# Optimization experiments

Measured on AMD Instinct MI355X. Metric: run time of the kernel, lower is better.

## Reference

```python
import jax, jax.numpy as jnp
import numpy as np

N = 30000      # nodes
E = 240000     # edges (before self-loops)
D = 128        # vec_dim
L = 6          # GAT layers
NEG_SLOPE = 0.2
EPS = 1e-5


def setup_inputs() -> dict:
    key = jax.random.key(0)
    ks = jax.random.split(key, 20)
    s = 1.0 / np.sqrt(D)
    inp = {
        "x": jax.random.randint(ks[0], (N,), 0, 120),
        "edge_index": jax.random.randint(ks[1], (2, E), 0, N),
        "emb": jax.random.normal(ks[2], (120, D), jnp.float32) * 0.05,
        # stacked GATv2Conv params for 6 layers (heads=1)
        "Wl": jax.random.normal(ks[3], (L, D, D), jnp.float32) * s,
        "bl": jnp.zeros((L, D), jnp.float32),
        "Wr": jax.random.normal(ks[4], (L, D, D), jnp.float32) * s,
        "br": jnp.zeros((L, D), jnp.float32),
        "att": jax.random.normal(ks[5], (L, D), jnp.float32) * s,
        "conv_bias": jnp.zeros((L, D), jnp.float32),
        # PyG LayerNorm (applied after layers 0..4)
        "ln_g": jnp.ones((L - 1, D), jnp.float32),
        "ln_b": jnp.zeros((L - 1, D), jnp.float32),
        # outer Linear + BatchNorm1d
        "lin_W": jax.random.normal(ks[6], (D, D), jnp.float32) * s,
        "lin_b": jnp.zeros((D,), jnp.float32),
        "bn_g": jnp.ones((D,), jnp.float32),
        "bn_b": jnp.zeros((D,), jnp.float32),
    }
    return inp


def _segment_softmax(score, seg, num_segments):
    # numerically stable softmax over variable-degree neighborhoods
    m = jax.ops.segment_max(score, seg, num_segments=num_segments)
    ex = jnp.exp(score - m[seg])
    denom = jax.ops.segment_sum(ex, seg, num_segments=num_segments)
    return ex / denom[seg]


def _gat_forward(h, src, dst, Wl, bl, Wr, br, att, conv_bias, ln_g, ln_b):
    xg = h
    for i in range(L):
        xl = xg @ Wl[i] + bl[i]          # [N, D] source transform
        xr = xg @ Wr[i] + br[i]          # [N, D] target transform
        # GATv2 attention: a^T LeakyReLU(x_l[j] + x_r[i]) per edge j->i
        e = jax.nn.leaky_relu(xl[src] + xr[dst], NEG_SLOPE)   # [E2, D]
        score = e @ att[i]                                     # [E2]
        alpha = _segment_softmax(score, dst, N)                # [E2]
        msg = alpha[:, None] * xl[src]                         # [E2, D]
        xg = jax.ops.segment_sum(msg, dst, num_segments=N) + conv_bias[i]
        if i < L - 1:
            # PyG LayerNorm(mode='graph'): global mean/std, per-channel affine
            mu = xg.mean()
            var = ((xg - mu) ** 2).mean()
            xg = (xg - mu) / jnp.sqrt(var + EPS) * ln_g[i] + ln_b[i]
            xg = jax.nn.relu(xg)
            # dropout(0.1) is identity in eval mode
    return xg


def reference(x, edge_index, emb, Wl, bl, Wr, br, att, conv_bias,
              ln_g, ln_b, lin_W, lin_b, bn_g, bn_b):
    h = emb[x]                                      # [N, D]
    # PyG GATv2Conv default add_self_loops=True
    loops = jnp.arange(N, dtype=edge_index.dtype)
    src = jnp.concatenate([edge_index[0], loops])   # [E2]
    dst = jnp.concatenate([edge_index[1], loops])   # [E2]
    xg = _gat_forward(h, src, dst, Wl, bl, Wr, br, att, conv_bias, ln_g, ln_b)
    out = (h + xg) @ lin_W + lin_b                  # [N, D]
    # BatchNorm1d (batch-statistics / train-mode math)
    mu = out.mean(axis=0)
    var = out.var(axis=0)
    out = (out - mu) / jnp.sqrt(var + EPS) * bn_g + bn_b
    return out
```

## Files before the change

### kernel.cpp

```cpp
#include <hip/hip_runtime.h>
#include <math.h>

#define N_NODES 30000
#define N_EDGES 240000
#define E2 (N_EDGES + N_NODES)
#define D 128
#define LAYERS 6
#define NEG_SLOPE 0.2f
#define LN_EPS 1e-5f

typedef unsigned short u16;
typedef unsigned int u32;
using bfrag = __attribute__((ext_vector_type(8))) short;
using f32x4 = __attribute__((ext_vector_type(4))) float;

__device__ inline u16 f2bf(float f) {
    u32 u = __float_as_uint(f);
    u32 r = u + 0x7fffu + ((u >> 16) & 1u);
    return (u16)(r >> 16);
}
__device__ inline u32 pack2(float a, float b) { return (u32)f2bf(a) | ((u32)f2bf(b) << 16); }
__device__ inline float bflo(u32 u) { return __uint_as_float(u << 16); }
__device__ inline float bfhi(u32 u) { return __uint_as_float(u & 0xffff0000u); }
__device__ inline u32 bfadd2(u32 a, u32 b) {
    return pack2(bflo(a) + bflo(b), bfhi(a) + bfhi(b));
}

__device__ inline float red8_dpp(float x) {
    x += __int_as_float(__builtin_amdgcn_update_dpp(0, __float_as_int(x), 0xB1, 0xF, 0xF, true));
    x += __int_as_float(__builtin_amdgcn_update_dpp(0, __float_as_int(x), 0x4E, 0xF, 0xF, true));
    x += __int_as_float(__builtin_amdgcn_update_dpp(0, __float_as_int(x), 0x141, 0xF, 0xF, true));
    return x;
}

__global__ __launch_bounds__(256) void wt_convert(const float* __restrict__ Wl,
        const float* __restrict__ Wr, const float* __restrict__ linW, u16* __restrict__ wt)
{
    __shared__ u16 tile[128 * 129];
    int b = blockIdx.x;
    const float* src = (b == 12) ? linW
                     : ((b & 1) ? Wr + (size_t)(b >> 1) * 16384 : Wl + (size_t)(b >> 1) * 16384);
    int t = threadIdx.x;
    #pragma unroll 4
    for (int i = 0; i < 64; i++) {
        int idx = t + 256 * i;
        int k = idx >> 7, n = idx & 127;
        tile[n * 129 + k] = f2bf(src[idx]);
    }
    __syncthreads();
    u16* dst = wt + (size_t)b * 16384;
    #pragma unroll 4
    for (int i = 0; i < 64; i++) {
        int idx = t + 256 * i;
        int n = idx >> 7, k = idx & 127;
        dst[idx] = tile[n * 129 + k];
    }
}

__global__ __launch_bounds__(256) void hist_kernel(const int* __restrict__ ei, int* __restrict__ cnt)
{
    int e = blockIdx.x * 256 + threadIdx.x;
    if (e >= E2) return;
    int d = (e < N_EDGES) ? ei[N_EDGES + e] : (e - N_EDGES);
    atomicAdd(&cnt[d], 1);
}

__global__ __launch_bounds__(1024) void scan1_kernel(const int* __restrict__ cnt,
        int* __restrict__ lscan, int* __restrict__ bsum)
{
    __shared__ int wtot[16];
    int t = threadIdx.x, lane = t & 63, w = t >> 6;
    int i = blockIdx.x * 1024 + t;
    int v = (i < N_NODES) ? cnt[i] : 0;
    int s = v;
    #pragma unroll
    for (int off = 1; off < 64; off <<= 1) {
        int u = __shfl_up(s, off);
        if (lane >= off) s += u;
    }
    if (lane == 63) wtot[w] = s;
    __syncthreads();
    if (t < 16) {
        int xv = wtot[t];
        #pragma unroll
        for (int off = 1; off < 16; off <<= 1) {
            int u = __shfl_up(xv, off);
            if (t >= off) xv += u;
        }
        wtot[t] = xv;
    }
    __syncthreads();
    int incl = ((w == 0) ? 0 : wtot[w - 1]) + s;
    if (i < N_NODES) lscan[i] = incl;
    if (t == 0) bsum[blockIdx.x] = wtot[15];
}

__global__ __launch_bounds__(1024) void scan3_kernel(const int* __restrict__ lscan,
        const int* __restrict__ bsum, const int* __restrict__ cnt,
        int* __restrict__ row_off, int* __restrict__ cursor)
{
    __shared__ int sboff;
    if (threadIdx.x < 64) {
        int v = (threadIdx.x < 30) ? bsum[threadIdx.x] : 0;
        int s = v;
        #pragma unroll
        for (int off = 1; off < 64; off <<= 1) {
            int u = __shfl_up(s, off);
            if ((int)threadIdx.x >= off) s += u;
        }
        if (threadIdx.x == blockIdx.x) sboff = s - v;
    }
    __syncthreads();
    int i = blockIdx.x * 1024 + threadIdx.x;
    if (i == 0) row_off[0] = 0;
    if (i < N_NODES) {
        int r = lscan[i] + sboff;
        row_off[i + 1] = r;
        cursor[i] = r - cnt[i];
    }
}

__global__ __launch_bounds__(256) void scatter_kernel(const int* __restrict__ ei,
        int* __restrict__ cursor, int* __restrict__ csr_src)
{
    int e = blockIdx.x * 256 + threadIdx.x;
    if (e >= E2) return;
    int s, d;
    if (e < N_EDGES) { s = ei[e]; d = ei[N_EDGES + e]; }
    else             { s = e - N_EDGES; d = s; }
    int pos = atomicAdd(&cursor[d], 1);
    csr_src[pos] = s;
}

template<bool LN, bool DUAL, bool OUTF, bool EMB>
__global__ __launch_bounds__(256) void gemm_mfma(
    const u16* __restrict__ Abf, const u16* __restrict__ A2bf,
    const float* __restrict__ Aln, const float* __restrict__ lnacc,
    const float* __restrict__ lng, const float* __restrict__ lnb,
    const int* __restrict__ xidx, const float* __restrict__ emb, u16* __restrict__ h_out,
    const u16* __restrict__ Wt1, const float* __restrict__ b1,
    float* __restrict__ C1f, u16* __restrict__ C1h,
    const u16* __restrict__ Wt2, const float* __restrict__ b2, u16* __restrict__ C2h,
    float* __restrict__ bnacc, int M)
{
    __shared__ u16 As[32 * 136];
    __shared__ float sLN[2];
    int t = threadIdx.x;
    int m0 = blockIdx.x * 32;
    int lane = t & 63, w = t >> 6;
    int n16 = lane & 15, quad = lane >> 4;
    int c0 = w * 32;

    bfrag bW1[2][4], bW2[2][4];
    #pragma unroll
    for (int c = 0; c < 2; c++)
        #pragma unroll
        for (int ks = 0; ks < 4; ks++)
            bW1[c][ks] = *(const bfrag*)(Wt1 + (size_t)(c0 + c * 16 + n16) * 128 + ks * 32 + quad * 8);
    if (DUAL) {
        #pragma unroll
        for (int c = 0; c < 2; c++)
            #pragma unroll
            for (int ks = 0; ks < 4; ks++)
                bW2[c][ks] = *(const bfrag*)(Wt2 + (size_t)(c0 + c * 16 + n16) * 128 + ks * 32 + quad * 8);
    }

    if (LN) {
        if (w == 0) {
            float2 v = ((const float2*)lnacc)[lane];
            float s = v.x, ss = v.y;
            #pragma unroll
            for (int off = 32; off > 0; off >>= 1) {
                s += __shfl_xor(s, off); ss += __shfl_xor(ss, off);
            }
            if (lane == 0) {
                const float invM = 1.f / ((float)N_NODES * (float)D);
                float mu  = s * invM;
                float var = ss * invM - mu * mu;
                sLN[0] = mu;
                sLN[1] = rsqrtf(var + LN_EPS);
            }
        }
        __syncthreads();
        float mu = sLN[0], inv = sLN[1];
        #pragma unroll
        for (int i = 0; i < 4; i++) {
            int idx = t + 256 * i;
            int row = idx >> 5, c4 = idx & 31;
            int gr = m0 + row;
            float4 v = make_float4(0.f, 0.f, 0.f, 0.f);
            if (gr < M) v = ((const float4*)(Aln + (size_t)gr * D))[c4];
            float4 gv = ((const float4*)lng)[c4];
            float4 bv = ((const float4*)lnb)[c4];
            v.x = (v.x - mu) * inv * gv.x + bv.x; v.x = v.x > 0.f ? v.x : 0.f;
            v.y = (v.y - mu) * inv * gv.y + bv.y; v.y = v.y > 0.f ? v.y : 0.f;
            v.z = (v.z - mu) * inv * gv.z + bv.z; v.z = v.z > 0.f ? v.z : 0.f;
            v.w = (v.w - mu) * inv * gv.w + bv.w; v.w = v.w > 0.f ? v.w : 0.f;
            uint2 pk = make_uint2(pack2(v.x, v.y), pack2(v.z, v.w));
            *(uint2*)&As[row * 136 + c4 * 4] = pk;
        }
    } else if (EMB) {
        #pragma unroll
        for (int i = 0; i < 2; i++) {
            int idx = t + 256 * i;
            int row = idx >> 4, c16 = idx & 15;
            int gr = m0 + row;
            uint4 v = make_uint4(0u, 0u, 0u, 0u);
            if (gr < M) {
                const float* er = emb + (size_t)xidx[gr] * D + c16 * 8;
                float4 e0 = ((const float4*)er)[0];
                float4 e1 = ((const float4*)er)[1];
                v.x = pack2(e0.x, e0.y); v.y = pack2(e0.z, e0.w);
                v.z = pack2(e1.x, e1.y); v.w = pack2(e1.z, e1.w);
                ((uint4*)(h_out + (size_t)gr * 128))[c16] = v;
            }
            *(uint4*)&As[row * 136 + c16 * 8] = v;
        }
    } else {
        #pragma unroll
        for (int i = 0; i < 2; i++) {
            int idx = t + 256 * i;
            int row = idx >> 4, c16 = idx & 15;
            int gr = m0 + row;
            uint4 v = make_uint4(0u, 0u, 0u, 0u);
            if (gr < M) {
                v = ((const uint4*)(Abf + (size_t)gr * 128))[c16];
                if (A2bf) {
                    uint4 u = ((const uint4*)(A2bf + (size_t)gr * 128))[c16];
                    v.x = bfadd2(v.x, u.x); v.y = bfadd2(v.y, u.y);
                    v.z = bfadd2(v.z, u.z); v.w = bfadd2(v.w, u.w);
                }
            }
            *(uint4*)&As[row * 136 + c16 * 8] = v;
        }
    }
    __syncthreads();

    f32x4 zero = {0.f, 0.f, 0.f, 0.f};
    f32x4 acc1[2][2] = {{zero, zero}, {zero, zero}};
    f32x4 acc2[2][2] = {{zero, zero}, {zero, zero}};
    #pragma unroll
    for (int ks = 0; ks < 4; ks++) {
        bfrag a[2];
        #pragma unroll
        for (int r = 0; r < 2; r++)
            a[r] = *(const bfrag*)&As[(r * 16 + n16) * 136 + ks * 32 + quad * 8];
        #pragma unroll
        for (int r = 0; r < 2; r++)
            #pragma unroll
            for (int c = 0; c < 2; c++) {
                acc1[r][c] = __builtin_amdgcn_mfma_f32_16x16x32_bf16(a[r], bW1[c][ks], acc1[r][c], 0, 0, 0);
                if (DUAL)
                    acc2[r][c] = __builtin_amdgcn_mfma_f32_16x16x32_bf16(a[r], bW2[c][ks], acc2[r][c], 0, 0, 0);
            }
    }

    float bv1[2] = { b1[c0 + n16], b1[c0 + 16 + n16] };
    float bns[2] = {0.f, 0.f}, bnss[2] = {0.f, 0.f};
    #pragma unroll
    for (int r = 0; r < 2; r++)
        #pragma unroll
        for (int c = 0; c < 2; c++)
            #pragma unroll
            for (int reg = 0; reg < 4; reg++) {
                int grow = m0 + r * 16 + quad * 4 + reg;
                if (grow < M) {
                    float val = acc1[r][c][reg] + bv1[c];
                    int col = c0 + c * 16 + n16;
                    if (OUTF) {
                        C1f[(size_t)grow * 128 + col] = val;
                        bns[c] += val; bnss[c] += val * val;
                    } else {
                        C1h[(size_t)grow * 128 + col] = f2bf(val);
                    }
                }
            }
    if (OUTF) {
        #pragma unroll
        for (int c = 0; c < 2; c++) {
            #pragma unroll
            for (int msk = 16; msk <= 32; msk <<= 1) {
                bns[c]  += __shfl_xor(bns[c], msk);
                bnss[c] += __shfl_xor(bnss[c], msk);
            }
        }
        if (quad == 0) {
            float* base = bnacc + (size_t)(blockIdx.x & 15) * 256;
            #pragma unroll
            for (int c = 0; c < 2; c++) {
                int col = c0 + c * 16 + n16;
                atomicAdd(&base[col], bns[c]);
                atomicAdd(&base[128 + col], bnss[c]);
            }
        }
    }
    if (DUAL) {
        float bv2[2] = { b2[c0 + n16], b2[c0 + 16 + n16] };
        #pragma unroll
        for (int r = 0; r < 2; r++)
            #pragma unroll
            for (int c = 0; c < 2; c++)
                #pragma unroll
                for (int reg = 0; reg < 4; reg++) {
                    int grow = m0 + r * 16 + quad * 4 + reg;
                    if (grow < M)
                        C2h[(size_t)grow * 128 + c0 + c * 16 + n16] = f2bf(acc2[r][c][reg] + bv2[c]);
                }
    }
}

__global__ __launch_bounds__(256) void gat_agg(
    const u16* __restrict__ xl, const u16* __restrict__ xr,
    const int* __restrict__ row_off, const int* __restrict__ csr_src,
    const float* __restrict__ att, const float* __restrict__ conv_bias,
    float* __restrict__ xg, u16* __restrict__ xg_bf, float* __restrict__ lnacc)
{
    int wave = threadIdx.x >> 6, lane = threadIdx.x & 63;
    int node = blockIdx.x * 4 + wave;
    int g = lane >> 3, q = lane & 7;

    const uint4* xrow = (const uint4*)(xr + (size_t)node * 128);
    uint4 rrA = xrow[2 * q], rrB = xrow[2 * q + 1];
    float4 r0 = make_float4(bflo(rrA.x), bfhi(rrA.x), bflo(rrA.y), bfhi(rrA.y));
    float4 r1 = make_float4(bflo(rrA.z), bfhi(rrA.z), bflo(rrA.w), bfhi(rrA.w));
    float4 r2 = make_float4(bflo(rrB.x), bfhi(rrB.x), bflo(rrB.y), bfhi(rrB.y));
    float4 r3 = make_float4(bflo(rrB.z), bfhi(rrB.z), bflo(rrB.w), bfhi(rrB.w));
    float4 av0 = ((const float4*)att)[4 * q];
    float4 av1 = ((const float4*)att)[4 * q + 1];
    float4 av2 = ((const float4*)att)[4 * q + 2];
    float4 av3 = ((const float4*)att)[4 * q + 3];

    int s0 = row_off[node], s1 = row_off[node + 1];
    float denom = 0.f;
    float4 a0 = make_float4(0.f, 0.f, 0.f, 0.f), a1 = a0, a2 = a0, a3 = a0;

    #pragma unroll 2
    for (int s = s0 + g; s < s1; s += 8) {
        int src = csr_src[s];
        const uint4* row = (const uint4*)(xl + (size_t)src * 128);
        uint4 rawA = row[2 * q], rawB = row[2 * q + 1];
        float4 v0 = make_float4(bflo(rawA.x), bfhi(rawA.x), bflo(rawA.y), bfhi(rawA.y));
        float4 v1 = make_float4(bflo(rawA.z), bfhi(rawA.z), bflo(rawA.w), bfhi(rawA.w));
        float4 v2 = make_float4(bflo(rawB.x), bfhi(rawB.x), bflo(rawB.y), bfhi(rawB.y));
        float4 v3 = make_float4(bflo(rawB.z), bfhi(rawB.z), bflo(rawB.w), bfhi(rawB.w));
        float pr = 0.f, tt;
        tt = v0.x + r0.x; tt = tt > 0.f ? tt : NEG_SLOPE * tt; pr += av0.x * tt;
        tt = v0.y + r0.y; tt = tt > 0.f ? tt : NEG_SLOPE * tt; pr += av0.y * tt;
        tt = v0.z + r0.z; tt = tt > 0.f ? tt : NEG_SLOPE * tt; pr += av0.z * tt;
        tt = v0.w + r0.w; tt = tt > 0.f ? tt : NEG_SLOPE * tt; pr += av0.w * tt;
        tt = v1.x + r1.x; tt = tt > 0.f ? tt : NEG_SLOPE * tt; pr += av1.x * tt;
        tt = v1.y + r1.y; tt = tt > 0.f ? tt : NEG_SLOPE * tt; pr += av1.y * tt;
        tt = v1.z + r1.z; tt = tt > 0.f ? tt : NEG_SLOPE * tt; pr += av1.z * tt;
        tt = v1.w + r1.w; tt = tt > 0.f ? tt : NEG_SLOPE * tt; pr += av1.w * tt;
        tt = v2.x + r2.x; tt = tt > 0.f ? tt : NEG_SLOPE * tt; pr += av2.x * tt;
        tt = v2.y + r2.y; tt = tt > 0.f ? tt : NEG_SLOPE * tt; pr += av2.y * tt;
        tt = v2.z + r2.z; tt = tt > 0.f ? tt : NEG_SLOPE * tt; pr += av2.z * tt;
        tt = v2.w + r2.w; tt = tt > 0.f ? tt : NEG_SLOPE * tt; pr += av2.w * tt;
        tt = v3.x + r3.x; tt = tt > 0.f ? tt : NEG_SLOPE * tt; pr += av3.x * tt;
        tt = v3.y + r3.y; tt = tt > 0.f ? tt : NEG_SLOPE * tt; pr += av3.y * tt;
        tt = v3.z + r3.z; tt = tt > 0.f ? tt : NEG_SLOPE * tt; pr += av3.z * tt;
        tt = v3.w + r3.w; tt = tt > 0.f ? tt : NEG_SLOPE * tt; pr += av3.w * tt;
        pr = red8_dpp(pr);
        float wv = __expf(pr);
        denom += wv;
        a0.x += wv * v0.x; a0.y += wv * v0.y; a0.z += wv * v0.z; a0.w += wv * v0.w;
        a1.x += wv * v1.x; a1.y += wv * v1.y; a1.z += wv * v1.z; a1.w += wv * v1.w;
        a2.x += wv * v2.x; a2.y += wv * v2.y; a2.z += wv * v2.z; a2.w += wv * v2.w;
        a3.x += wv * v3.x; a3.y += wv * v3.y; a3.z += wv * v3.z; a3.w += wv * v3.w;
    }

    #pragma unroll
    for (int msk = 8; msk <= 32; msk <<= 1) {
        denom += __shfl_xor(denom, msk);
        a0.x += __shfl_xor(a0.x, msk); a0.y += __shfl_xor(a0.y, msk);
        a0.z += __shfl_xor(a0.z, msk); a0.w += __shfl_xor(a0.w, msk);
        a1.x += __shfl_xor(a1.x, msk); a1.y += __shfl_xor(a1.y, msk);
        a1.z += __shfl_xor(a1.z, msk); a1.w += __shfl_xor(a1.w, msk);
        a2.x += __shfl_xor(a2.x, msk); a2.y += __shfl_xor(a2.y, msk);
        a2.z += __shfl_xor(a2.z, msk); a2.w += __shfl_xor(a2.w, msk);
        a3.x += __shfl_xor(a3.x, msk); a3.y += __shfl_xor(a3.y, msk);
        a3.z += __shfl_xor(a3.z, msk); a3.w += __shfl_xor(a3.w, msk);
    }

    float4 cb0 = ((const float4*)conv_bias)[4 * q];
    float4 cb1 = ((const float4*)conv_bias)[4 * q + 1];
    float4 cb2 = ((const float4*)conv_bias)[4 * q + 2];
    float4 cb3 = ((const float4*)conv_bias)[4 * q + 3];
    float inv = 1.f / denom;
    float4 o0, o1, o2, o3;
    o0.x = a0.x * inv + cb0.x; o0.y = a0.y * inv + cb0.y;
    o0.z = a0.z * inv + cb0.z; o0.w = a0.w * inv + cb0.w;
    o1.x = a1.x * inv + cb1.x; o1.y = a1.y * inv + cb1.y;
    o1.z = a1.z * inv + cb1.z; o1.w = a1.w * inv + cb1.w;
    o2.x = a2.x * inv + cb2.x; o2.y = a2.y * inv + cb2.y;
    o2.z = a2.z * inv + cb2.z; o2.w = a2.w * inv + cb2.w;
    o3.x = a3.x * inv + cb3.x; o3.y = a3.y * inv + cb3.y;
    o3.z = a3.z * inv + cb3.z; o3.w = a3.w * inv + cb3.w;

    if (xg_bf) {
        if (g == 0) {
            uint4 pk0 = make_uint4(pack2(o0.x, o0.y), pack2(o0.z, o0.w),
                                   pack2(o1.x, o1.y), pack2(o1.z, o1.w));
            uint4 pk1 = make_uint4(pack2(o2.x, o2.y), pack2(o2.z, o2.w),
                                   pack2(o3.x, o3.y), pack2(o3.z, o3.w));
            ((uint4*)(xg_bf + (size_t)node * 128))[2 * q]     = pk0;
            ((uint4*)(xg_bf + (size_t)node * 128))[2 * q + 1] = pk1;
        }
    } else {
        if (g == 0) {
            float4* od = (float4*)(xg + (size_t)node * 128);
            od[4 * q] = o0; od[4 * q + 1] = o1; od[4 * q + 2] = o2; od[4 * q + 3] = o3;
        }
        float s  = o0.x + o0.y + o0.z + o0.w + o1.x + o1.y + o1.z + o1.w
                 + o2.x + o2.y + o2.z + o2.w + o3.x + o3.y + o3.z + o3.w;
        float ss = o0.x*o0.x + o0.y*o0.y + o0.z*o0.z + o0.w*o0.w
                 + o1.x*o1.x + o1.y*o1.y + o1.z*o1.z + o1.w*o1.w
                 + o2.x*o2.x + o2.y*o2.y + o2.z*o2.z + o2.w*o2.w
                 + o3.x*o3.x + o3.y*o3.y + o3.z*o3.z + o3.w*o3.w;
        s  = red8_dpp(s);
        ss = red8_dpp(ss);
        __shared__ float sred[8];
        if (lane == 0) { sred[wave] = s; sred[4 + wave] = ss; }
        __syncthreads();
        if (threadIdx.x == 0) {
            int slot = blockIdx.x & 63;
            atomicAdd(&lnacc[2 * slot],     sred[0] + sred[1] + sred[2] + sred[3]);
            atomicAdd(&lnacc[2 * slot + 1], sred[4] + sred[5] + sred[6] + sred[7]);
        }
    }
}

__global__ __launch_bounds__(256) void bn_apply(float* __restrict__ out, const float* __restrict__ acc,
        const float* __restrict__ g, const float* __restrict__ b)
{
    int idx = blockIdx.x * 256 + threadIdx.x;
    if (idx >= N_NODES * 32) return;
    int c4 = idx & 31;
    float4 s1 = make_float4(0.f, 0.f, 0.f, 0.f), s2 = s1;
    #pragma unroll
    for (int slot = 0; slot < 16; slot++) {
        float4 a = ((const float4*)(acc + slot * 256))[c4];
        float4 d = ((const float4*)(acc + slot * 256 + 128))[c4];
        s1.x += a.x; s1.y += a.y; s1.z += a.z; s1.w += a.w;
        s2.x += d.x; s2.y += d.y; s2.z += d.z; s2.w += d.w;
    }
    float4 gv = ((const float4*)g)[c4];
    float4 bv = ((const float4*)b)[c4];
    float4 v = ((float4*)out)[idx];
    const float invN = 1.f / (float)N_NODES;
    float mu, var, inv;
    mu = s1.x * invN; var = s2.x * invN - mu * mu; inv = rsqrtf(var + LN_EPS);
    v.x = (v.x - mu) * inv * gv.x + bv.x;
    mu = s1.y * invN; var = s2.y * invN - mu * mu; inv = rsqrtf(var + LN_EPS);
    v.y = (v.y - mu) * inv * gv.y + bv.y;
    mu = s1.z * invN; var = s2.z * invN - mu * mu; inv = rsqrtf(var + LN_EPS);
    v.z = (v.z - mu) * inv * gv.z + bv.z;
    mu = s1.w * invN; var = s2.w * invN - mu * mu; inv = rsqrtf(var + LN_EPS);
    v.w = (v.w - mu) * inv * gv.w + bv.w;
    ((float4*)out)[idx] = v;
}

extern "C" void kernel_launch(void* const* d_in, const int* in_sizes, int n_in,
                              void* d_out, int out_size, void* d_ws, size_t ws_size,
                              hipStream_t stream)
{
    const int*   x    = (const int*)d_in[0];
    const int*   ei   = (const int*)d_in[1];
    const float* emb  = (const float*)d_in[2];
    const float* Wl   = (const float*)d_in[3];
    const float* bl   = (const float*)d_in[4];
    const float* Wr   = (const float*)d_in[5];
    const float* br   = (const float*)d_in[6];
    const float* att  = (const float*)d_in[7];
    const float* cbias= (const float*)d_in[8];
    const float* lng  = (const float*)d_in[9];
    const float* lnb  = (const float*)d_in[10];
    const float* linW = (const float*)d_in[11];
    const float* linb = (const float*)d_in[12];
    const float* bng  = (const float*)d_in[13];
    const float* bnb  = (const float*)d_in[14];
    float* out = (float*)d_out;

    char* p = (char*)d_ws;
    float* xg    = (float*)p; p += (size_t)N_NODES * D * 4;
    u16*   xl_bf = (u16*)p;   p += (size_t)N_NODES * D * 2;
    u16*   xr_bf = (u16*)p;   p += (size_t)N_NODES * D * 2;
    u16*   xg_bf = (u16*)p;   p += (size_t)N_NODES * D * 2;
    u16*   h_bf  = (u16*)p;   p += (size_t)N_NODES * D * 2;
    u16*   wt    = (u16*)p;   p += (size_t)13 * 16384 * 2;
    int* cnt     = (int*)p; p += ((N_NODES * 4 + 255) / 256) * 256;
    int* lscan   = (int*)p; p += ((N_NODES * 4 + 255) / 256) * 256;
    int* row_off = (int*)p; p += (((N_NODES + 1) * 4 + 255) / 256) * 256;
    int* cursor  = (int*)p; p += ((N_NODES * 4 + 255) / 256) * 256;
    int* csr_src = (int*)p; p += ((E2 * 4 + 255) / 256) * 256;
    int* bsum    = (int*)p; p += 256;
    float* accs  = (float*)p; p += 20480;

    hipMemsetAsync(cnt, 0, N_NODES * 4, stream);
    hipMemsetAsync(accs, 0, (640 + 4096) * 4, stream);

    wt_convert<<<13, 256, 0, stream>>>(Wl, Wr, linW, wt);
    hist_kernel<<<(E2 + 255) / 256, 256, 0, stream>>>(ei, cnt);
    scan1_kernel<<<30, 1024, 0, stream>>>(cnt, lscan, bsum);
    scan3_kernel<<<30, 1024, 0, stream>>>(lscan, bsum, cnt, row_off, cursor);
    scatter_kernel<<<(E2 + 255) / 256, 256, 0, stream>>>(ei, cursor, csr_src);

    for (int i = 0; i < LAYERS; i++) {
        if (i == 0) {
            gemm_mfma<false, true, false, true><<<938, 256, 0, stream>>>(
                nullptr, nullptr, nullptr, nullptr, nullptr, nullptr,
                x, emb, h_bf,
                wt + (size_t)0 * 16384, bl + 0, nullptr, xl_bf,
                wt + (size_t)1 * 16384, br + 0, xr_bf, nullptr, N_NODES);
        } else {
            gemm_mfma<true, true, false, false><<<938, 256, 0, stream>>>(
                nullptr, nullptr, xg, accs + (i - 1) * 128,
                lng + (size_t)(i - 1) * D, lnb + (size_t)(i - 1) * D,
                nullptr, nullptr, nullptr,
                wt + (size_t)(2 * i) * 16384, bl + i * D, nullptr, xl_bf,
                wt + (size_t)(2 * i + 1) * 16384, br + i * D, xr_bf, nullptr, N_NODES);
        }
        gat_agg<<<7500, 256, 0, stream>>>(xl_bf, xr_bf, row_off, csr_src,
            att + i * D, cbias + i * D, xg,
            (i == LAYERS - 1) ? xg_bf : nullptr,
            (i < LAYERS - 1) ? (accs + i * 128) : nullptr);
    }
    gemm_mfma<false, false, true, false><<<938, 256, 0, stream>>>(
        xg_bf, h_bf, nullptr, nullptr, nullptr, nullptr,
        nullptr, nullptr, nullptr,
        wt + (size_t)12 * 16384, linb, out, nullptr,
        nullptr, nullptr, nullptr, accs + 640, N_NODES);
    bn_apply<<<3750, 256, 0, stream>>>(out, accs + 640, bng, bnb);
}
```

Before: 581.0 us.

## Enlarge GEMM row tile to 128 and process 4 edges per wave in GAT aggregation

The GEMM kernel now processes 128 rows per block instead of 32, so each block's register-resident weight fragments are reused across four times as many rows and the grid shrinks to about 235 blocks. Launch bounds are set to 2 blocks per SM. Separately, the aggregation kernel is reorganised so each edge's 128-dim row is handled by 16 lanes holding 8 channels each, giving 4 edges in flight per wave instead of 8 lanes and 8 edges. The dot-product reduction widens to 16 lanes to match. The trade-offs are more accumulator registers and fewer GEMM blocks, which risks underfilling the GPU, while aggregation gets more memory-level parallelism per lane.

Result: no change. 585.2 us (+0.7%).

```diff
diff --git a/kernel.cpp b/kernel.cpp
--- a/kernel.cpp
+++ b/kernel.cpp
@@ -26,10 +26,11 @@
     return pack2(bflo(a) + bflo(b), bfhi(a) + bfhi(b));
 }
 
-__device__ inline float red8_dpp(float x) {
+__device__ inline float red16_dpp(float x) {
     x += __int_as_float(__builtin_amdgcn_update_dpp(0, __float_as_int(x), 0xB1, 0xF, 0xF, true));
     x += __int_as_float(__builtin_amdgcn_update_dpp(0, __float_as_int(x), 0x4E, 0xF, 0xF, true));
     x += __int_as_float(__builtin_amdgcn_update_dpp(0, __float_as_int(x), 0x141, 0xF, 0xF, true));
+    x += __int_as_float(__builtin_amdgcn_update_dpp(0, __float_as_int(x), 0x140, 0xF, 0xF, true));
     return x;
 }
 
@@ -133,7 +134,7 @@
 }
 
 template<bool LN, bool DUAL, bool OUTF, bool EMB>
-__global__ __launch_bounds__(256) void gemm_mfma(
+__global__ __launch_bounds__(256, 2) void gemm_mfma(
     const u16* __restrict__ Abf, const u16* __restrict__ A2bf,
     const float* __restrict__ Aln, const float* __restrict__ lnacc,
     const float* __restrict__ lng, const float* __restrict__ lnb,
@@ -143,10 +144,10 @@
     const u16* __restrict__ Wt2, const float* __restrict__ b2, u16* __restrict__ C2h,
     float* __restrict__ bnacc, int M)
 {
-    __shared__ u16 As[32 * 136];
+    __shared__ u16 As[128 * 136];
     __shared__ float sLN[2];
     int t = threadIdx.x;
-    int m0 = blockIdx.x * 32;
+    int m0 = blockIdx.x * 128;
     int lane = t & 63, w = t >> 6;
     int n16 = lane & 15, quad = lane >> 4;
     int c0 = w * 32;
@@ -184,7 +185,7 @@
         __syncthreads();
         float mu = sLN[0], inv = sLN[1];
         #pragma unroll
-        for (int i = 0; i < 4; i++) {
+        for (int i = 0; i < 16; i++) {
             int idx = t + 256 * i;
             int row = idx >> 5, c4 = idx & 31;
             int gr = m0 + row;
@@ -201,7 +202,7 @@
         }
     } else if (EMB) {
         #pragma unroll
-        for (int i = 0; i < 2; i++) {
+        for (int i = 0; i < 8; i++) {
             int idx = t + 256 * i;
             int row = idx >> 4, c16 = idx & 15;
             int gr = m0 + row;
@@ -218,7 +219,7 @@
         }
     } else {
         #pragma unroll
-        for (int i = 0; i < 2; i++) {
+        for (int i = 0; i < 8; i++) {
             int idx = t + 256 * i;
             int row = idx >> 4, c16 = idx & 15;
             int gr = m0 + row;
@@ -237,16 +238,20 @@
     __syncthreads();
 
     f32x4 zero = {0.f, 0.f, 0.f, 0.f};
-    f32x4 acc1[2][2] = {{zero, zero}, {zero, zero}};
-    f32x4 acc2[2][2] = {{zero, zero}, {zero, zero}};
+    f32x4 acc1[8][2], acc2[8][2];
+    #pragma unroll
+    for (int r = 0; r < 8; r++)
+        #pragma unroll
+        for (int c = 0; c < 2; c++) { acc1[r][c] = zero; if (DUAL) acc2[r][c] = zero; }
+
     #pragma unroll
     for (int ks = 0; ks < 4; ks++) {
-        bfrag a[2];
-        #pragma unroll
-        for (int r = 0; r < 2; r++)
+        bfrag a[8];
+        #pragma unroll
+        for (int r = 0; r < 8; r++)
             a[r] = *(const bfrag*)&As[(r * 16 + n16) * 136 + ks * 32 + quad * 8];
         #pragma unroll
-        for (int r = 0; r < 2; r++)
+        for (int r = 0; r < 8; r++)
             #pragma unroll
             for (int c = 0; c < 2; c++) {
                 acc1[r][c] = __builtin_amdgcn_mfma_f32_16x16x32_bf16(a[r], bW1[c][ks], acc1[r][c], 0, 0, 0);
@@ -258,7 +263,7 @@
     float bv1[2] = { b1[c0 + n16], b1[c0 + 16 + n16] };
     float bns[2] = {0.f, 0.f}, bnss[2] = {0.f, 0.f};
     #pragma unroll
-    for (int r = 0; r < 2; r++)
+    for (int r = 0; r < 8; r++)
         #pragma unroll
         for (int c = 0; c < 2; c++)
             #pragma unroll
@@ -297,7 +302,7 @@
     if (DUAL) {
         float bv2[2] = { b2[c0 + n16], b2[c0 + 16 + n16] };
         #pragma unroll
-        for (int r = 0; r < 2; r++)
+        for (int r = 0; r < 8; r++)
             #pragma unroll
             for (int c = 0; c < 2; c++)
                 #pragma unroll
@@ -317,32 +322,24 @@
 {
     int wave = threadIdx.x >> 6, lane = threadIdx.x & 63;
     int node = blockIdx.x * 4 + wave;
-    int g = lane >> 3, q = lane & 7;
-
-    const uint4* xrow = (const uint4*)(xr + (size_t)node * 128);
-    uint4 rrA = xrow[2 * q], rrB = xrow[2 * q + 1];
-    float4 r0 = make_float4(bflo(rrA.x), bfhi(rrA.x), bflo(rrA.y), bfhi(rrA.y));
-    float4 r1 = make_float4(bflo(rrA.z), bfhi(rrA.z), bflo(rrA.w), bfhi(rrA.w));
-    float4 r2 = make_float4(bflo(rrB.x), bfhi(rrB.x), bflo(rrB.y), bfhi(rrB.y));
-    float4 r3 = make_float4(bflo(rrB.z), bfhi(rrB.z), bflo(rrB.w), bfhi(rrB.w));
-    float4 av0 = ((const float4*)att)[4 * q];
-    float4 av1 = ((const float4*)att)[4 * q + 1];
-    float4 av2 = ((const float4*)att)[4 * q + 2];
-    float4 av3 = ((const float4*)att)[4 * q + 3];
+    int g = lane >> 4, q = lane & 15;
+
+    uint4 rr = *(const uint4*)(xr + (size_t)node * 128 + q * 8);
+    float4 r0 = make_float4(bflo(rr.x), bfhi(rr.x), bflo(rr.y), bfhi(rr.y));
+    float4 r1 = make_float4(bflo(rr.z), bfhi(rr.z), bflo(rr.w), bfhi(rr.w));
+    float4 av0 = ((const float4*)att)[2 * q];
+    float4 av1 = ((const float4*)att)[2 * q + 1];
 
     int s0 = row_off[node], s1 = row_off[node + 1];
     float denom = 0.f;
-    float4 a0 = make_float4(0.f, 0.f, 0.f, 0.f), a1 = a0, a2 = a0, a3 = a0;
-
-    #pragma unroll 2
-    for (int s = s0 + g; s < s1; s += 8) {
+    float4 a0 = make_float4(0.f, 0.f, 0.f, 0.f), a1 = a0;
+
+    #pragma unroll 4
+    for (int s = s0 + g; s < s1; s += 4) {
         int src = csr_src[s];
-        const uint4* row = (const uint4*)(xl + (size_t)src * 128);
-        uint4 rawA = row[2 * q], rawB = row[2 * q + 1];
-        float4 v0 = make_float4(bflo(rawA.x), bfhi(rawA.x), bflo(rawA.y), bfhi(rawA.y));
-        float4 v1 = make_float4(bflo(rawA.z), bfhi(rawA.z), bflo(rawA.w), bfhi(rawA.w));
-        float4 v2 = make_float4(bflo(rawB.x), bfhi(rawB.x), bflo(rawB.y), bfhi(rawB.y));
-        float4 v3 = make_float4(bflo(rawB.z), bfhi(rawB.z), bflo(rawB.w), bfhi(rawB.w));
+        uint4 raw = *(const uint4*)(xl + (size_t)src * 128 + q * 8);
+        float4 v0 = make_float4(bflo(raw.x), bfhi(raw.x), bflo(raw.y), bfhi(raw.y));
+        float4 v1 = make_float4(bflo(raw.z), bfhi(raw.z), bflo(raw.w), bfhi(raw.w));
         float pr = 0.f, tt;
         tt = v0.x + r0.x; tt = tt > 0.f ? tt : NEG_SLOPE * tt; pr += av0.x * tt;
         tt = v0.y + r0.y; tt = tt > 0.f ? tt : NEG_SLOPE * tt; pr += av0.y * tt;
@@ -352,73 +349,47 @@
         tt = v1.y + r1.y; tt = tt > 0.f ? tt : NEG_SLOPE * tt; pr += av1.y * tt;
         tt = v1.z + r1.z; tt = tt > 0.f ? tt : NEG_SLOPE * tt; pr += av1.z * tt;
         tt = v1.w + r1.w; tt = tt > 0.f ? tt : NEG_SLOPE * tt; pr += av1.w * tt;
-        tt = v2.x + r2.x; tt = tt > 0.f ? tt : NEG_SLOPE * tt; pr += av2.x * tt;
-        tt = v2.y + r2.y; tt = tt > 0.f ? tt : NEG_SLOPE * tt; pr += av2.y * tt;
-        tt = v2.z + r2.z; tt = tt > 0.f ? tt : NEG_SLOPE * tt; pr += av2.z * tt;
-        tt = v2.w + r2.w; tt = tt > 0.f ? tt : NEG_SLOPE * tt; pr += av2.w * tt;
-        tt = v3.x + r3.x; tt = tt > 0.f ? tt : NEG_SLOPE * tt; pr += av3.x * tt;
-        tt = v3.y + r3.y; tt = tt > 0.f ? tt : NEG_SLOPE * tt; pr += av3.y * tt;
-        tt = v3.z + r3.z; tt = tt > 0.f ? tt : NEG_SLOPE * tt; pr += av3.z * tt;
-        tt = v3.w + r3.w; tt = tt > 0.f ? tt : NEG_SLOPE * tt; pr += av3.w * tt;
-        pr = red8_dpp(pr);
+        pr = red16_dpp(pr);
         float wv = __expf(pr);
         denom += wv;
         a0.x += wv * v0.x; a0.y += wv * v0.y; a0.z += wv * v0.z; a0.w += wv * v0.w;
         a1.x += wv * v1.x; a1.y += wv * v1.y; a1.z += wv * v1.z; a1.w += wv * v1.w;
-        a2.x += wv * v2.x; a2.y += wv * v2.y; a2.z += wv * v2.z; a2.w += wv * v2.w;
-        a3.x += wv * v3.x; a3.y += wv * v3.y; a3.z += wv * v3.z; a3.w += wv * v3.w;
-    }
-
-    #pragma unroll
-    for (int msk = 8; msk <= 32; msk <<= 1) {
+    }
+
+    #pragma unroll
+    for (int msk = 16; msk <= 32; msk <<= 1) {
         denom += __shfl_xor(denom, msk);
         a0.x += __shfl_xor(a0.x, msk); a0.y += __shfl_xor(a0.y, msk);
         a0.z += __shfl_xor(a0.z, msk); a0.w += __shfl_xor(a0.w, msk);
         a1.x += __shfl_xor(a1.x, msk); a1.y += __shfl_xor(a1.y, msk);
         a1.z += __shfl_xor(a1.z, msk); a1.w += __shfl_xor(a1.w, msk);
-        a2.x += __shfl_xor(a2.x, msk); a2.y += __shfl_xor(a2.y, msk);
-        a2.z += __shfl_xor(a2.z, msk); a2.w += __shfl_xor(a2.w, msk);
-        a3.x += __shfl_xor(a3.x, msk); a3.y += __shfl_xor(a3.y, msk);
-        a3.z += __shfl_xor(a3.z, msk); a3.w += __shfl_xor(a3.w, msk);
-    }
-
-    float4 cb0 = ((const float4*)conv_bias)[4 * q];
-    float4 cb1 = ((const float4*)conv_bias)[4 * q + 1];
-    float4 cb2 = ((const float4*)conv_bias)[4 * q + 2];
-    float4 cb3 = ((const float4*)conv_bias)[4 * q + 3];
+    }
+
+    float4 cb0 = ((const float4*)conv_bias)[2 * q];
+    float4 cb1 = ((const float4*)conv_bias)[2 * q + 1];
     float inv = 1.f / denom;
-    float4 o0, o1, o2, o3;
+    float4 o0, o1;
     o0.x = a0.x * inv + cb0.x; o0.y = a0.y * inv + cb0.y;
     o0.z = a0.z * inv + cb0.z; o0.w = a0.w * inv + cb0.w;
     o1.x = a1.x * inv + cb1.x; o1.y = a1.y * inv + cb1.y;
     o1.z = a1.z * inv + cb1.z; o1.w = a1.w * inv + cb1.w;
-    o2.x = a2.x * inv + cb2.x; o2.y = a2.y * inv + cb2.y;
-    o2.z = a2.z * inv + cb2.z; o2.w = a2.w * inv + cb2.w;
-    o3.x = a3.x * inv + cb3.x; o3.y = a3.y * inv + cb3.y;
-    o3.z = a3.z * inv + cb3.z; o3.w = a3.w * inv + cb3.w;
 
     if (xg_bf) {
         if (g == 0) {
-            uint4 pk0 = make_uint4(pack2(o0.x, o0.y), pack2(o0.z, o0.w),
-                                   pack2(o1.x, o1.y), pack2(o1.z, o1.w));
-            uint4 pk1 = make_uint4(pack2(o2.x, o2.y), pack2(o2.z, o2.w),
-                                   pack2(o3.x, o3.y), pack2(o3.z, o3.w));
-            ((uint4*)(xg_bf + (size_t)node * 128))[2 * q]     = pk0;
-            ((uint4*)(xg_bf + (size_t)node * 128))[2 * q + 1] = pk1;
+            uint4 pk = make_uint4(pack2(o0.x, o0.y), pack2(o0.z, o0.w),
+                                  pack2(o1.x, o1.y), pack2(o1.z, o1.w));
+            ((uint4*)(xg_bf + (size_t)node * 128))[q] = pk;
         }
     } else {
         if (g == 0) {
-            float4* od = (float4*)(xg + (size_t)node * 128);
-            od[4 * q] = o0; od[4 * q + 1] = o1; od[4 * q + 2] = o2; od[4 * q + 3] = o3;
-        }
-        float s  = o0.x + o0.y + o0.z + o0.w + o1.x + o1.y + o1.z + o1.w
-                 + o2.x + o2.y + o2.z + o2.w + o3.x + o3.y + o3.z + o3.w;
+            ((float4*)(xg + (size_t)node * 128))[2 * q]     = o0;
+            ((float4*)(xg + (size_t)node * 128))[2 * q + 1] = o1;
+        }
+        float s  = o0.x + o0.y + o0.z + o0.w + o1.x + o1.y + o1.z + o1.w;
         float ss = o0.x*o0.x + o0.y*o0.y + o0.z*o0.z + o0.w*o0.w
-                 + o1.x*o1.x + o1.y*o1.y + o1.z*o1.z + o1.w*o1.w
-                 + o2.x*o2.x + o2.y*o2.y + o2.z*o2.z + o2.w*o2.w
-                 + o3.x*o3.x + o3.y*o3.y + o3.z*o3.z + o3.w*o3.w;
-        s  = red8_dpp(s);
-        ss = red8_dpp(ss);
+                 + o1.x*o1.x + o1.y*o1.y + o1.z*o1.z + o1.w*o1.w;
+        s  = red16_dpp(s);
+        ss = red16_dpp(ss);
         __shared__ float sred[8];
         if (lane == 0) { sred[wave] = s; sred[4 + wave] = ss; }
         __syncthreads();
@@ -505,15 +476,16 @@
     scan3_kernel<<<30, 1024, 0, stream>>>(lscan, bsum, cnt, row_off, cursor);
     scatter_kernel<<<(E2 + 255) / 256, 256, 0, stream>>>(ei, cursor, csr_src);
 
+    const int GEMM_GRID = (N_NODES + 127) / 128;
     for (int i = 0; i < LAYERS; i++) {
         if (i == 0) {
-            gemm_mfma<false, true, false, true><<<938, 256, 0, stream>>>(
+            gemm_mfma<false, true, false, true><<<GEMM_GRID, 256, 0, stream>>>(
                 nullptr, nullptr, nullptr, nullptr, nullptr, nullptr,
                 x, emb, h_bf,
                 wt + (size_t)0 * 16384, bl + 0, nullptr, xl_bf,
                 wt + (size_t)1 * 16384, br + 0, xr_bf, nullptr, N_NODES);
         } else {
-            gemm_mfma<true, true, false, false><<<938, 256, 0, stream>>>(
+            gemm_mfma<true, true, false, false><<<GEMM_GRID, 256, 0, stream>>>(
                 nullptr, nullptr, xg, accs + (i - 1) * 128,
                 lng + (size_t)(i - 1) * D, lnb + (size_t)(i - 1) * D,
                 nullptr, nullptr, nullptr,
@@ -525,7 +497,7 @@
             (i == LAYERS - 1) ? xg_bf : nullptr,
             (i < LAYERS - 1) ? (accs + i * 128) : nullptr);
     }
-    gemm_mfma<false, false, true, false><<<938, 256, 0, stream>>>(
+    gemm_mfma<false, false, true, false><<<GEMM_GRID, 256, 0, stream>>>(
         xg_bf, h_bf, nullptr, nullptr, nullptr, nullptr,
         nullptr, nullptr, nullptr,
         wt + (size_t)12 * 16384, linb, out, nullptr,
```
